# Kernel optimization log

Measured on AMD Instinct MI355X. Metric: run time of the kernel, lower is better.

The kernel has to match this reference:

```python
import jax, jax.numpy as jnp
import numpy as np
import math

LOG2PI = math.log(2.0 * math.pi)
NEG = -1e20


def gaussian_loglik(z, mean, log_std):
    tmp = (z - mean) * jnp.exp(-log_std)
    return -0.5 * (tmp * tmp + 2.0 * log_std + LOG2PI)


def setup_inputs() -> dict:
    key = jax.random.key(0)
    k1, k2 = jax.random.split(key)
    N, T, D = 16, 2048, 2
    # event arrival times, increasing along T
    input_time = jnp.sort(jax.random.uniform(k1, (N, T, 1), dtype=jnp.float32), axis=1)
    input_loc = jax.random.normal(k2, (N, T, D), dtype=jnp.float32)
    return {
        "input_time": input_time,
        "input_loc": input_loc,
        "mu0": jnp.asarray(0.0, jnp.float32),
        "logstd0": jnp.asarray(0.0, jnp.float32),
        "coeff_decay": jnp.asarray(0.1, jnp.float32),
        "spatial_logstd": jnp.asarray(0.1, jnp.float32),
    }


def reference(input_time, input_loc, mu0, logstd0, coeff_decay, spatial_logstd):
    N, T, _ = input_time.shape
    # base log-likelihood of the first event location under N(mu0, exp(logstd0))
    s0 = input_loc[:, 0]                                   # (N, D)
    loglik0 = gaussian_loglik(s0, mu0, logstd0).sum(-1)    # (N,)

    # pairwise time differences dt[n,i,j] = t[n,i] - t[n,j]
    dt = input_time - jnp.swapaxes(input_time, 1, 2)       # (N, T, T)

    # pairwise spatial Gaussian log-likelihoods, summed over D
    pw = gaussian_loglik(
        input_loc[:, :, None, :],                          # (N, T, 1, D)
        input_loc[:, None, :, :],                          # (N, 1, T, D)
        spatial_logstd,
    ).sum(-1)                                              # (N, T, T)

    # causal mask: keep strictly-lower triangle, fill rest with -1e20
    mask = jnp.tril(jnp.ones((T, T), dtype=bool), k=-1)
    pw = jnp.where(mask, pw, NEG)

    dt_logdecay = jnp.where(mask, -dt / jax.nn.softplus(coeff_decay), NEG)
    dt_logdecay = dt_logdecay - jax.nn.logsumexp(dt_logdecay, axis=-1, keepdims=True)

    loglik = jax.nn.logsumexp(pw + dt_logdecay, axis=-1)   # (N, T)
    return jnp.concatenate([loglik0[:, None], loglik[:, 1:]], axis=1)
```

## Files before the change

### kernel.cpp

```cpp
#include <hip/hip_runtime.h>
#include <math.h>

#define TT     2048
#define LOG2E  1.4426950408889634f
#define LN2    0.6931471805599453f
#define LOG2PI 1.8378770664093453f

__global__ __launch_bounds__(256) void gmsm_pack(
    const float* __restrict__ time,
    const float* __restrict__ loc,
    const float* __restrict__ coeffp,
    const float* __restrict__ lsp,
    float4* __restrict__ packed,
    int total)
{
    const int idx = blockIdx.x * 256 + threadIdx.x;
    if (idx >= total) return;
    const float sp = log1pf(expf(*coeffp));
    const float ss = LOG2E / sp;
    const float ls = *lsp;
    const float c1 = -0.5f * expf(-2.0f * ls) * LOG2E;

    const float t   = time[idx];
    const float2 xy = ((const float2*)loc)[idx];
    const float bt  = t * ss;
    const float r   = fmaf(xy.x, xy.x, xy.y * xy.y);
    float4 o;
    o.x = xy.x;
    o.y = xy.y;
    o.z = fmaf(r, c1, bt);
    o.w = __builtin_amdgcn_exp2f(bt);
    packed[idx] = o;
}

__global__ __launch_bounds__(512) void gmsm_main(
    const float4* __restrict__ packed,
    const float* __restrict__ mu0p,
    const float* __restrict__ logstd0p,
    const float* __restrict__ lsp,
    float* __restrict__ out,
    int nrowblk)
{
    const int b    = blockIdx.x;
    const int half = nrowblk >> 1;
    const int g    = (b < half) ? (b << 1) : ((((nrowblk - 1) - b) << 1) | 1);
    const int n    = g >> 5;
    const int base = (g & 31) << 6;

    const int tid  = threadIdx.x;
    const int lane = tid & 63;
    const int w    = __builtin_amdgcn_readfirstlane(tid >> 6);

    const float4* __restrict__ pk = packed + (size_t)n * TT;

    const float ls   = *lsp;
    const float m2c1 = expf(-2.0f * ls) * LOG2E;
    const float4 pi  = pk[base + lane];
    const float u    = m2c1 * pi.x;
    const float v    = m2c1 * pi.y;

    float s_q = 0.0f;
    float s_b = 0.0f;
    const int cfull = base >> 6;

    for (int c = w; c < cfull; c += 8) {
        const float4* cp = pk + (c << 6);
        #pragma unroll 8
        for (int jj = 0; jj < 64; ++jj) {
            const float4 f = cp[jj];
            s_q += __builtin_amdgcn_exp2f(fmaf(u, f.x, fmaf(v, f.y, f.z)));
            s_b += f.w;
        }
    }
    if (w == (cfull & 7)) {
        const float4* cp = pk + base;
        for (int jj = 0; jj < 63; ++jj) {
            const float4 f = cp[jj];
            const float e = __builtin_amdgcn_exp2f(fmaf(u, f.x, fmaf(v, f.y, f.z)));
            const bool on = jj < lane;
            s_q += on ? e   : 0.0f;
            s_b += on ? f.w : 0.0f;
        }
    }

    __shared__ float ldsq[8 * 64];
    __shared__ float ldsb[8 * 64];
    ldsq[tid] = s_q;
    ldsb[tid] = s_b;
    __syncthreads();

    if (tid < 64) {
        float q = 0.0f, bsum = 0.0f;
        #pragma unroll
        for (int k = 0; k < 8; ++k) {
            q    += ldsq[(k << 6) | tid];
            bsum += ldsb[(k << 6) | tid];
        }
        const int i = base + tid;
        float res;
        if (i == 0) {
            const float mu0 = *mu0p, l0 = *logstd0p;
            const float inv = expf(-l0);
            const float4 p0 = pk[0];
            const float tx = (p0.x - mu0) * inv;
            const float ty = (p0.y - mu0) * inv;
            res = -0.5f * (tx * tx + ty * ty + 4.0f * l0 + 2.0f * LOG2PI);
        } else {
            const float c1 = -0.5f * m2c1;
            const float c0 = -(2.0f * ls + LOG2PI);
            const float4 pr = pk[i];
            const float r  = fmaf(pr.x, pr.x, pr.y * pr.y);
            res = fmaf(__builtin_amdgcn_logf(q) - __builtin_amdgcn_logf(bsum)
                       + c1 * r, LN2, c0);
        }
        out[(size_t)n * TT + i] = res;
    }
}

extern "C" void kernel_launch(void* const* d_in, const int* in_sizes, int n_in,
                              void* d_out, int out_size, void* d_ws, size_t ws_size,
                              hipStream_t stream) {
    const float* time   = (const float*)d_in[0];
    const float* loc    = (const float*)d_in[1];
    const float* mu0    = (const float*)d_in[2];
    const float* logstd = (const float*)d_in[3];
    const float* coeff  = (const float*)d_in[4];
    const float* sls    = (const float*)d_in[5];
    float* out = (float*)d_out;

    const int nrows = out_size;
    const int nrowblk = nrows >> 6;
    float4* packed = (float4*)d_ws;

    gmsm_pack<<<(nrows + 255) / 256, 256, 0, stream>>>(time, loc, coeff, sls,
                                                       packed, nrows);
    gmsm_main<<<nrowblk, 512, 0, stream>>>(packed, mu0, logstd, sls, out, nrowblk);
}
```

Baseline: 79.52 us.

## Fuse pack kernel into main kernel and stage packed rows in LDS

Removes the separate packing kernel. Each block now recomputes the packed float4 (loc, scaled time plus radial term, exp2 of time) for the prefix of its sequence it needs, stores it in shared memory, and runs the pairwise loop from LDS instead of global memory. This drops one launch and the global round trip through the workspace. The cost is redundant packing work in every block, since later row blocks repack up to 2048 elements, plus 32KB of LDS per block that may limit occupancy.

```diff
diff --git a/kernel.cpp b/kernel.cpp
--- a/kernel.cpp
+++ b/kernel.cpp
@@ -6,41 +6,20 @@
 #define LN2    0.6931471805599453f
 #define LOG2PI 1.8378770664093453f
 
-__global__ __launch_bounds__(256) void gmsm_pack(
+__global__ __launch_bounds__(512) void gmsm_fused(
     const float* __restrict__ time,
     const float* __restrict__ loc,
-    const float* __restrict__ coeffp,
-    const float* __restrict__ lsp,
-    float4* __restrict__ packed,
-    int total)
-{
-    const int idx = blockIdx.x * 256 + threadIdx.x;
-    if (idx >= total) return;
-    const float sp = log1pf(expf(*coeffp));
-    const float ss = LOG2E / sp;
-    const float ls = *lsp;
-    const float c1 = -0.5f * expf(-2.0f * ls) * LOG2E;
-
-    const float t   = time[idx];
-    const float2 xy = ((const float2*)loc)[idx];
-    const float bt  = t * ss;
-    const float r   = fmaf(xy.x, xy.x, xy.y * xy.y);
-    float4 o;
-    o.x = xy.x;
-    o.y = xy.y;
-    o.z = fmaf(r, c1, bt);
-    o.w = __builtin_amdgcn_exp2f(bt);
-    packed[idx] = o;
-}
-
-__global__ __launch_bounds__(512) void gmsm_main(
-    const float4* __restrict__ packed,
     const float* __restrict__ mu0p,
     const float* __restrict__ logstd0p,
+    const float* __restrict__ coeffp,
     const float* __restrict__ lsp,
     float* __restrict__ out,
     int nrowblk)
 {
+    __shared__ float4 pkl[TT];
+    __shared__ float  ldsq[512];
+    __shared__ float  ldsb[512];
+
     const int b    = blockIdx.x;
     const int half = nrowblk >> 1;
     const int g    = (b < half) ? (b << 1) : ((((nrowblk - 1) - b) << 1) | 1);
@@ -51,20 +30,35 @@
     const int lane = tid & 63;
     const int w    = __builtin_amdgcn_readfirstlane(tid >> 6);
 
-    const float4* __restrict__ pk = packed + (size_t)n * TT;
-
+    const float sp   = log1pf(expf(*coeffp));
+    const float ss   = LOG2E / sp;
     const float ls   = *lsp;
     const float m2c1 = expf(-2.0f * ls) * LOG2E;
-    const float4 pi  = pk[base + lane];
-    const float u    = m2c1 * pi.x;
-    const float v    = m2c1 * pi.y;
+    const float c1   = -0.5f * m2c1;
+
+    const int J = base + 64;
+    const float* tp = time + (size_t)n * TT;
+    const float2* lp = (const float2*)(loc + (size_t)n * TT * 2);
+    for (int e = tid; e < J; e += 512) {
+        const float  t  = tp[e];
+        const float2 xy = lp[e];
+        const float  bt = t * ss;
+        const float  r  = fmaf(xy.x, xy.x, xy.y * xy.y);
+        pkl[e] = make_float4(xy.x, xy.y, fmaf(r, c1, bt),
+                             __builtin_amdgcn_exp2f(bt));
+    }
+    __syncthreads();
+
+    const float4 pi = pkl[base + lane];
+    const float u = m2c1 * pi.x;
+    const float v = m2c1 * pi.y;
 
     float s_q = 0.0f;
     float s_b = 0.0f;
     const int cfull = base >> 6;
 
     for (int c = w; c < cfull; c += 8) {
-        const float4* cp = pk + (c << 6);
+        const float4* cp = &pkl[c << 6];
         #pragma unroll 8
         for (int jj = 0; jj < 64; ++jj) {
             const float4 f = cp[jj];
@@ -73,7 +67,7 @@
         }
     }
     if (w == (cfull & 7)) {
-        const float4* cp = pk + base;
+        const float4* cp = &pkl[base];
         for (int jj = 0; jj < 63; ++jj) {
             const float4 f = cp[jj];
             const float e = __builtin_amdgcn_exp2f(fmaf(u, f.x, fmaf(v, f.y, f.z)));
@@ -83,35 +77,31 @@
         }
     }
 
-    __shared__ float ldsq[8 * 64];
-    __shared__ float ldsb[8 * 64];
     ldsq[tid] = s_q;
     ldsb[tid] = s_b;
     __syncthreads();
 
     if (tid < 64) {
-        float q = 0.0f, bsum = 0.0f;
+        float q = 0.0f, bs = 0.0f;
         #pragma unroll
         for (int k = 0; k < 8; ++k) {
-            q    += ldsq[(k << 6) | tid];
-            bsum += ldsb[(k << 6) | tid];
+            q  += ldsq[(k << 6) | tid];
+            bs += ldsb[(k << 6) | tid];
         }
         const int i = base + tid;
         float res;
         if (i == 0) {
             const float mu0 = *mu0p, l0 = *logstd0p;
             const float inv = expf(-l0);
-            const float4 p0 = pk[0];
+            const float4 p0 = pkl[0];
             const float tx = (p0.x - mu0) * inv;
             const float ty = (p0.y - mu0) * inv;
             res = -0.5f * (tx * tx + ty * ty + 4.0f * l0 + 2.0f * LOG2PI);
         } else {
-            const float c1 = -0.5f * m2c1;
-            const float c0 = -(2.0f * ls + LOG2PI);
-            const float4 pr = pk[i];
+            const float4 pr = pkl[i];
             const float r  = fmaf(pr.x, pr.x, pr.y * pr.y);
-            res = fmaf(__builtin_amdgcn_logf(q) - __builtin_amdgcn_logf(bsum)
-                       + c1 * r, LN2, c0);
+            res = fmaf(__builtin_amdgcn_logf(q) - __builtin_amdgcn_logf(bs)
+                       + c1 * r, LN2, -(2.0f * ls + LOG2PI));
         }
         out[(size_t)n * TT + i] = res;
     }
@@ -128,11 +118,9 @@
     const float* sls    = (const float*)d_in[5];
     float* out = (float*)d_out;
 
-    const int nrows = out_size;
+    const int nrows   = out_size;
     const int nrowblk = nrows >> 6;
-    float4* packed = (float4*)d_ws;
 
-    gmsm_pack<<<(nrows + 255) / 256, 256, 0, stream>>>(time, loc, coeff, sls,
-                                                       packed, nrows);
-    gmsm_main<<<nrowblk, 512, 0, stream>>>(packed, mu0, logstd, sls, out, nrowblk);
+    gmsm_fused<<<nrowblk, 512, 0, stream>>>(time, loc, mu0, logstd, coeff, sls,
+                                            out, nrowblk);
 }
```

Measured after the change: 71.83 us. -9.7%, faster.
